# Optimization experiments

Hardware: AMD Instinct MI355X
Metric: run time of the kernel (lower is better)

## Reference

```python
import jax, jax.numpy as jnp
import numpy as np

B, H, W, C = 8, 64, 64, 64
C8 = C // 8

def setup_inputs() -> dict:
    key = jax.random.key(0)
    ks = jax.random.split(key, 5)
    x = jax.random.normal(ks[0], (B, H, W, C), dtype=jnp.float32)
    # 1x1 conv kernels (fan-in scaled) + biases
    wq = jax.random.normal(ks[1], (C, C8), dtype=jnp.float32) / np.sqrt(C)
    wk = jax.random.normal(ks[2], (C, C8), dtype=jnp.float32) / np.sqrt(C)
    wv = jax.random.normal(ks[3], (C, C), dtype=jnp.float32) / np.sqrt(C)
    bq = jnp.zeros((C8,), dtype=jnp.float32)
    bk = jnp.zeros((C8,), dtype=jnp.float32)
    bv = jnp.zeros((C,), dtype=jnp.float32)
    gamma = jax.random.normal(ks[4], (), dtype=jnp.float32)
    return {"x": x, "wq": wq, "bq": bq, "wk": wk, "bk": bk,
            "wv": wv, "bv": bv, "gamma": gamma}

def reference(x, wq, bq, wk, bk, wv, bv, gamma):
    b, h, w, c = x.shape
    n = h * w
    # 1x1 convs == per-pixel linear projections
    q = (jnp.einsum('bhwc,cd->bhwd', x, wq) + bq).reshape(b, n, -1)  # [B,N,C/8]
    k = (jnp.einsum('bhwc,cd->bhwd', x, wk) + bk).reshape(b, n, -1)  # [B,N,C/8]
    v = (jnp.einsum('bhwc,cd->bhwd', x, wv) + bv).reshape(b, n, -1)  # [B,N,C]
    # Unscaled attention: softmax over keys (last axis), no 1/sqrt(d)
    attn = jax.nn.softmax(jnp.einsum('bnd,bmd->bnm', q, k), axis=-1)  # [B,N,N]
    out = jnp.einsum('bnm,bmc->bnc', attn, v).reshape(b, h, w, c)
    return out * gamma + x
```

## Files before the change

kernel.cpp:

```cpp
#include <hip/hip_runtime.h>
#include <hip/hip_bf16.h>


#define BB 8
#define NN 4096
#define CC 64
#define PSTRIDE 72
#define LOG2E 1.44269504088896f

typedef _Float16 f16;
typedef _Float16 half8 __attribute__((ext_vector_type(8)));
typedef _Float16 half4 __attribute__((ext_vector_type(4)));
typedef __fp16 fp16x2 __attribute__((ext_vector_type(2)));
typedef float floatx4 __attribute__((ext_vector_type(4)));

static __device__ inline half4 pack4(float a, float b, float c, float d) {
    fp16x2 lo = __builtin_amdgcn_cvt_pkrtz(a, b);
    fp16x2 hi = __builtin_amdgcn_cvt_pkrtz(c, d);
    unsigned int lou = __builtin_bit_cast(unsigned int, lo);
    unsigned int hiu = __builtin_bit_cast(unsigned int, hi);
    unsigned long long packed = (unsigned long long)lou | ((unsigned long long)hiu << 32);
    return __builtin_bit_cast(half4, packed);
}


__global__ __launch_bounds__(256) void proj_all_kernel(
    const float* __restrict__ x,
    const float* __restrict__ wq, const float* __restrict__ bq,
    const float* __restrict__ wk, const float* __restrict__ bk,
    const float* __restrict__ wv, const float* __restrict__ bv,
    f16* __restrict__ Qh, f16* __restrict__ Kf, f16* __restrict__ Vf,
    float* __restrict__ qn2, float* __restrict__ kn2)
{
    __shared__ alignas(16) f16 Ws[80][PSTRIDE];
    __shared__ float Bs[80];
    __shared__ alignas(16) f16 Vs[64][68];
    __shared__ alignas(16) f16 Ks[64][12];
    const int tid = threadIdx.x;

    for (int i = tid; i < 4096; i += 256) {
        int cin = i >> 6, cout = i & 63;
        Ws[cout][cin] = (f16)wv[i];
    }
    for (int i = tid; i < 512; i += 256) {
        int cin = i >> 3, c = i & 7;
        Ws[64 + c][cin] = (f16)(wq[i] * LOG2E);
        Ws[72 + c][cin] = (f16)wk[i];
    }
    if (tid < 80)
        Bs[tid] = (tid < 64) ? bv[tid]
                : (tid < 72 ? bq[tid - 64] * LOG2E : bk[tid - 72]);
    __syncthreads();

    const int wave = tid >> 6, lane = tid & 63;
    const int quad = lane >> 4, n16 = lane & 15;
    const long pb = (long)blockIdx.x * 64;
    const long p0 = pb + wave * 16;
    const int  b   = (int)(pb >> 12);
    const int  nnb = (int)(pb & 4095);

    half8 ax[2];
#pragma unroll
    for (int kh = 0; kh < 2; ++kh) {
        const float* xp = x + (p0 + n16) * 64 + kh * 32 + quad * 8;
        float4 x1 = *(const float4*)xp;
        float4 x2 = *(const float4*)(xp + 4);
        ax[kh][0] = (f16)x1.x; ax[kh][1] = (f16)x1.y;
        ax[kh][2] = (f16)x1.z; ax[kh][3] = (f16)x1.w;
        ax[kh][4] = (f16)x2.x; ax[kh][5] = (f16)x2.y;
        ax[kh][6] = (f16)x2.z; ax[kh][7] = (f16)x2.w;
    }

#pragma unroll
    for (int ct = 0; ct < 5; ++ct) {
        const int cout = (ct < 4) ? ct * 16 + n16 : 64 + n16;
        const float bias = Bs[cout];
        half8 b0 = *(const half8*)(&Ws[cout][quad * 8]);
        half8 b1 = *(const half8*)(&Ws[cout][32 + quad * 8]);
        floatx4 acc = {bias, bias, bias, bias};
        acc = __builtin_amdgcn_mfma_f32_16x16x32_f16(ax[0], b0, acc, 0, 0, 0);
        acc = __builtin_amdgcn_mfma_f32_16x16x32_f16(ax[1], b1, acc, 0, 0, 0);
        if (ct < 4) {
#pragma unroll
            for (int r = 0; r < 4; ++r)
                Vs[wave * 16 + quad * 4 + r][ct * 16 + n16] = (f16)acc[r];
        } else {
            float n2[4];
#pragma unroll
            for (int r = 0; r < 4; ++r) n2[r] = acc[r] * acc[r];
#pragma unroll
            for (int d = 1; d < 8; d <<= 1)
#pragma unroll
                for (int r = 0; r < 4; ++r) n2[r] += __shfl_xor(n2[r], d, 64);
            if (n16 == 0) {
#pragma unroll
                for (int r = 0; r < 4; ++r) qn2[p0 + quad * 4 + r] = n2[r];
            } else if (n16 == 8) {
#pragma unroll
                for (int r = 0; r < 4; ++r) kn2[p0 + quad * 4 + r] = n2[r];
            }
            if (n16 < 8) {
                f16* dst = Qh + (p0 + quad * 4) * 8 + n16;
#pragma unroll
                for (int r = 0; r < 4; ++r) dst[r * 8] = (f16)acc[r];
            } else {
#pragma unroll
                for (int r = 0; r < 4; ++r)
                    Ks[wave * 16 + quad * 4 + r][n16 - 8] = (f16)acc[r];
            }
        }
    }
    __syncthreads();

#pragma unroll
    for (int u = 0; u < 2; ++u) {
        const int tt = wave * 2 + u;
        const int kb = tt >> 2, ct = tt & 3;
        half8 v;
#pragma unroll
        for (int j = 0; j < 4; ++j)
            v[j] = Vs[kb * 32 + quad * 4 + j][ct * 16 + n16];
#pragma unroll
        for (int j = 0; j < 4; ++j)
            v[4 + j] = Vs[kb * 32 + 16 + quad * 4 + j][ct * 16 + n16];
        const size_t kbg = (size_t)b * 128 + (nnb >> 5) + kb;
        *(half8*)(Vf + (kbg * 4 + ct) * 512 + lane * 8) = v;
    }
    if (wave < 2) {
        half8 kp;
#pragma unroll
        for (int e = 0; e < 2; ++e) {
            const int t = wave * 2 + e;
#pragma unroll
            for (int j = 0; j < 4; ++j) {
                f16 v = (f16)0.f;
                if (quad < 2) v = Ks[t * 16 + n16][quad * 4 + j];
                else if (quad == 2 && j == 0) v = (f16)1.f;
                kp[e * 4 + j] = v;
            }
        }
        const size_t kpg = (size_t)b * 128 + (nnb >> 5) + wave;
        *(half8*)(Kf + kpg * 512 + lane * 8) = kp;
    }
}

__global__ __launch_bounds__(256) void knorm_max_kernel(
    const float* __restrict__ kn2, float* __restrict__ Mk2)
{
    __shared__ float red[4];
    const int b = blockIdx.x, tid = threadIdx.x;
    float mx = 0.f;
    for (int i = tid; i < NN; i += 256) mx = fmaxf(mx, kn2[(size_t)b * NN + i]);
#pragma unroll
    for (int d = 1; d < 64; d <<= 1) mx = fmaxf(mx, __shfl_xor(mx, d, 64));
    if ((tid & 63) == 0) red[tid >> 6] = mx;
    __syncthreads();
    if (tid == 0) Mk2[b] = fmaxf(fmaxf(red[0], red[1]), fmaxf(red[2], red[3]));
}

__global__ __launch_bounds__(256, 2) void attn_kernel(
    const f16* __restrict__ Qh, const f16* __restrict__ Kf,
    const f16* __restrict__ Vf,
    const float* __restrict__ qn2, const float* __restrict__ Mk2,
    const float* __restrict__ x, const float* __restrict__ gptr,
    float* __restrict__ out)
{
    __shared__ alignas(16) float Obuf[3 * 4 * 64 * 20];
    __shared__ float Ls[4][4][16];

    const int tid  = threadIdx.x;
    const int wave = tid >> 6, lane = tid & 63;
    const int quad = lane >> 4, n16 = lane & 15;
    const int ks = wave;

    const int b  = blockIdx.x & 7;
    const int qt = blockIdx.x >> 3;
    const size_t bN = (size_t)b * NN;

    const float mk2 = Mk2[b];

    half4 bq4[4];
#pragma unroll
    for (int qs = 0; qs < 4; ++qs) {
        const int q = qt * 64 + qs * 16 + n16;
        const float mf = __builtin_sqrtf(qn2[bN + q] * mk2) - 12.0f;
        half4 v = {0, 0, 0, 0};
        if (quad < 2)
            v = *(const half4*)(Qh + (bN + q) * 8 + quad * 4);
        else if (quad == 2)
            v[0] = (f16)(-mf);
        bq4[qs] = v;
    }

    floatx4 oacc[4][4];
#pragma unroll
    for (int qs = 0; qs < 4; ++qs)
#pragma unroll
        for (int ct = 0; ct < 4; ++ct) oacc[qs][ct] = (floatx4){0.f, 0.f, 0.f, 0.f};
    float l_loc[4] = {0.f, 0.f, 0.f, 0.f};

    const f16* kfb = Kf + ((size_t)b * 128 + ks * 32) * 512 + lane * 8;
    const f16* vfb = Vf + ((size_t)b * 128 + ks * 32) * 2048 + lane * 8;
    const floatx4 zero4 = {0.f, 0.f, 0.f, 0.f};

    half8 kkc0 = *(const half8*)(kfb + 0);
    half8 kkc1 = *(const half8*)(kfb + 512);

    for (int it = 0; it < 16; ++it) {
        half8 avp[2][4];
#pragma unroll
        for (int p = 0; p < 2; ++p)
#pragma unroll
            for (int ct = 0; ct < 4; ++ct)
                avp[p][ct] = *(const half8*)(vfb + ((size_t)(it * 2 + p) * 4 + ct) * 512);

        half4 ak[4];
        ak[0] = __builtin_shufflevector(kkc0, kkc0, 0, 1, 2, 3);
        ak[1] = __builtin_shufflevector(kkc0, kkc0, 4, 5, 6, 7);
        ak[2] = __builtin_shufflevector(kkc1, kkc1, 0, 1, 2, 3);
        ak[3] = __builtin_shufflevector(kkc1, kkc1, 4, 5, 6, 7);

        const int itn = (it < 15) ? it + 1 : 15;
        kkc0 = *(const half8*)(kfb + (size_t)itn * 1024);
        kkc1 = *(const half8*)(kfb + (size_t)itn * 1024 + 512);

#pragma unroll
        for (int qs = 0; qs < 4; ++qs) {
            floatx4 sf[4];
#pragma unroll
            for (int t = 0; t < 4; ++t)
                sf[t] = __builtin_amdgcn_mfma_f32_16x16x16f16(ak[t], bq4[qs], zero4, 0, 0, 0);

            half4 pk[4];
            float rst[4];
#pragma unroll
            for (int t = 0; t < 4; ++t) {
                float p0 = __builtin_exp2f(sf[t][0]);
                float p1 = __builtin_exp2f(sf[t][1]);
                float p2 = __builtin_exp2f(sf[t][2]);
                float p3 = __builtin_exp2f(sf[t][3]);
                rst[t] = (p0 + p1) + (p2 + p3);
                pk[t] = pack4(p0, p1, p2, p3);
            }
            l_loc[qs] += (rst[0] + rst[1]) + (rst[2] + rst[3]);

#pragma unroll
            for (int t = 0; t < 4; ++t) {
                const int p = t >> 1;
#pragma unroll
                for (int ct = 0; ct < 4; ++ct) {
                    half4 va = (t & 1)
                        ? __builtin_shufflevector(avp[p][ct], avp[p][ct], 4, 5, 6, 7)
                        : __builtin_shufflevector(avp[p][ct], avp[p][ct], 0, 1, 2, 3);
                    oacc[qs][ct] = __builtin_amdgcn_mfma_f32_16x16x16f16(va, pk[t], oacc[qs][ct], 0, 0, 0);
                }
            }
        }
    }

    float l_run[4];
#pragma unroll
    for (int qs = 0; qs < 4; ++qs) {
        float l = l_loc[qs];
        l += __shfl_xor(l, 16, 64);
        l += __shfl_xor(l, 32, 64);
        l_run[qs] = l;
    }

    __syncthreads();
    if (ks > 0) {
#pragma unroll
        for (int qs = 0; qs < 4; ++qs) {
            if (quad == 0) Ls[ks][qs][n16] = l_run[qs];
            float* ob = Obuf + (size_t)(((ks - 1) * 4 + qs) * 64 + lane) * 20;
#pragma unroll
            for (int ct = 0; ct < 4; ++ct)
                *(floatx4*)(ob + ct * 4) = oacc[qs][ct];
        }
    }
    __syncthreads();
    if (ks == 0) {
        const float g = gptr[0];
#pragma unroll
        for (int qs = 0; qs < 4; ++qs) {
            float l = l_run[qs];
#pragma unroll
            for (int p = 1; p < 4; ++p) {
                l += Ls[p][qs][n16];
                const float* ob = Obuf + (size_t)(((p - 1) * 4 + qs) * 64 + lane) * 20;
#pragma unroll
                for (int ct = 0; ct < 4; ++ct) {
                    floatx4 t = *(const floatx4*)(ob + ct * 4);
                    oacc[qs][ct] += t;
                }
            }
            const float scale = g / l;
            const int q = qt * 64 + qs * 16 + n16;
#pragma unroll
            for (int ct = 0; ct < 4; ++ct) {
                const size_t idx = (bN + q) * CC + ct * 16 + quad * 4;
                float4 xr = *(const float4*)(x + idx);
                float4 res;
                res.x = oacc[qs][ct][0] * scale + xr.x;
                res.y = oacc[qs][ct][1] * scale + xr.y;
                res.z = oacc[qs][ct][2] * scale + xr.z;
                res.w = oacc[qs][ct][3] * scale + xr.w;
                *(float4*)(out + idx) = res;
            }
        }
    }
}

extern "C" void kernel_launch(void* const* d_in, const int* in_sizes, int n_in,
                              void* d_out, int out_size, void* d_ws, size_t ws_size,
                              hipStream_t stream) {
    const float* x     = (const float*)d_in[0];
    const float* wq    = (const float*)d_in[1];
    const float* bq    = (const float*)d_in[2];
    const float* wk    = (const float*)d_in[3];
    const float* bk    = (const float*)d_in[4];
    const float* wv    = (const float*)d_in[5];
    const float* bv    = (const float*)d_in[6];
    const float* gamma = (const float*)d_in[7];
    float* out = (float*)d_out;

    f16* Qh = (f16*)d_ws;
    f16* Kf = Qh + (size_t)BB * NN * 8;
    f16* Vf = Kf + (size_t)BB * 128 * 512;
    float* qn2 = (float*)(Vf + (size_t)BB * 128 * 4 * 512);
    float* kn2 = qn2 + (size_t)BB * NN;
    float* Mk2 = kn2 + (size_t)BB * NN;

    proj_all_kernel<<<512, 256, 0, stream>>>(x, wq, bq, wk, bk, wv, bv,
                                             Qh, Kf, Vf, qn2, kn2);
    knorm_max_kernel<<<BB, 256, 0, stream>>>(kn2, Mk2);
    attn_kernel<<<BB * 64, 256, 0, stream>>>(Qh, Kf, Vf, qn2, Mk2, x, gamma, out);
}
```

Measured before the change: 131.0 us.

## Shrink attention block to 16 queries for higher occupancy and more blocks

Each attention block now handles 16 queries instead of 64, so the grid grows fourfold to 2048 blocks. Launch bounds rise to 8 blocks per SM, and the accumulator registers and shared reduction buffer shrink to match. The aim is better latency hiding through occupancy and a more even spread of work across CUs. The cost is that K and V are loaded from memory four times as often, since each K/V tile is now reused across only 16 queries instead of 64.

New measurement: 172.3 us. 31.5% more time.

```diff
diff --git a/kernel.cpp b/kernel.cpp
--- a/kernel.cpp
+++ b/kernel.cpp
@@ -158,15 +158,15 @@
     if (tid == 0) Mk2[b] = fmaxf(fmaxf(red[0], red[1]), fmaxf(red[2], red[3]));
 }
 
-__global__ __launch_bounds__(256, 2) void attn_kernel(
+__global__ __launch_bounds__(256, 8) void attn_kernel(
     const f16* __restrict__ Qh, const f16* __restrict__ Kf,
     const f16* __restrict__ Vf,
     const float* __restrict__ qn2, const float* __restrict__ Mk2,
     const float* __restrict__ x, const float* __restrict__ gptr,
     float* __restrict__ out)
 {
-    __shared__ alignas(16) float Obuf[3 * 4 * 64 * 20];
-    __shared__ float Ls[4][4][16];
+    __shared__ alignas(16) float Obuf[3 * 64 * 20];
+    __shared__ float Ls[4][16];
 
     const int tid  = threadIdx.x;
     const int wave = tid >> 6, lane = tid & 63;
@@ -179,25 +179,22 @@
 
     const float mk2 = Mk2[b];
 
-    half4 bq4[4];
-#pragma unroll
-    for (int qs = 0; qs < 4; ++qs) {
-        const int q = qt * 64 + qs * 16 + n16;
+    half4 bq4;
+    {
+        const int q = qt * 16 + n16;
         const float mf = __builtin_sqrtf(qn2[bN + q] * mk2) - 12.0f;
         half4 v = {0, 0, 0, 0};
         if (quad < 2)
             v = *(const half4*)(Qh + (bN + q) * 8 + quad * 4);
         else if (quad == 2)
             v[0] = (f16)(-mf);
-        bq4[qs] = v;
-    }
-
-    floatx4 oacc[4][4];
-#pragma unroll
-    for (int qs = 0; qs < 4; ++qs)
-#pragma unroll
-        for (int ct = 0; ct < 4; ++ct) oacc[qs][ct] = (floatx4){0.f, 0.f, 0.f, 0.f};
-    float l_loc[4] = {0.f, 0.f, 0.f, 0.f};
+        bq4 = v;
+    }
+
+    floatx4 oacc[4];
+#pragma unroll
+    for (int ct = 0; ct < 4; ++ct) oacc[ct] = (floatx4){0.f, 0.f, 0.f, 0.f};
+    float l_loc = 0.f;
 
     const f16* kfb = Kf + ((size_t)b * 128 + ks * 32) * 512 + lane * 8;
     const f16* vfb = Vf + ((size_t)b * 128 + ks * 32) * 2048 + lane * 8;
@@ -207,13 +204,6 @@
     half8 kkc1 = *(const half8*)(kfb + 512);
 
     for (int it = 0; it < 16; ++it) {
-        half8 avp[2][4];
-#pragma unroll
-        for (int p = 0; p < 2; ++p)
-#pragma unroll
-            for (int ct = 0; ct < 4; ++ct)
-                avp[p][ct] = *(const half8*)(vfb + ((size_t)(it * 2 + p) * 4 + ct) * 512);
-
         half4 ak[4];
         ak[0] = __builtin_shufflevector(kkc0, kkc0, 0, 1, 2, 3);
         ak[1] = __builtin_shufflevector(kkc0, kkc0, 4, 5, 6, 7);
@@ -225,88 +215,75 @@
         kkc1 = *(const half8*)(kfb + (size_t)itn * 1024 + 512);
 
 #pragma unroll
-        for (int qs = 0; qs < 4; ++qs) {
-            floatx4 sf[4];
-#pragma unroll
-            for (int t = 0; t < 4; ++t)
-                sf[t] = __builtin_amdgcn_mfma_f32_16x16x16f16(ak[t], bq4[qs], zero4, 0, 0, 0);
-
-            half4 pk[4];
-            float rst[4];
-#pragma unroll
-            for (int t = 0; t < 4; ++t) {
-                float p0 = __builtin_exp2f(sf[t][0]);
-                float p1 = __builtin_exp2f(sf[t][1]);
-                float p2 = __builtin_exp2f(sf[t][2]);
-                float p3 = __builtin_exp2f(sf[t][3]);
-                rst[t] = (p0 + p1) + (p2 + p3);
-                pk[t] = pack4(p0, p1, p2, p3);
-            }
-            l_loc[qs] += (rst[0] + rst[1]) + (rst[2] + rst[3]);
-
-#pragma unroll
-            for (int t = 0; t < 4; ++t) {
-                const int p = t >> 1;
+        for (int p = 0; p < 2; ++p) {
+            half8 av[4];
+#pragma unroll
+            for (int ct = 0; ct < 4; ++ct)
+                av[ct] = *(const half8*)(vfb + ((size_t)(it * 2 + p) * 4 + ct) * 512);
+
+#pragma unroll
+            for (int e = 0; e < 2; ++e) {
+                const int t = p * 2 + e;
+                floatx4 sf = __builtin_amdgcn_mfma_f32_16x16x16f16(ak[t], bq4, zero4, 0, 0, 0);
+                float p0 = __builtin_exp2f(sf[0]);
+                float p1 = __builtin_exp2f(sf[1]);
+                float p2 = __builtin_exp2f(sf[2]);
+                float p3 = __builtin_exp2f(sf[3]);
+                l_loc += (p0 + p1) + (p2 + p3);
+                half4 pk = pack4(p0, p1, p2, p3);
 #pragma unroll
                 for (int ct = 0; ct < 4; ++ct) {
-                    half4 va = (t & 1)
-                        ? __builtin_shufflevector(avp[p][ct], avp[p][ct], 4, 5, 6, 7)
-                        : __builtin_shufflevector(avp[p][ct], avp[p][ct], 0, 1, 2, 3);
-                    oacc[qs][ct] = __builtin_amdgcn_mfma_f32_16x16x16f16(va, pk[t], oacc[qs][ct], 0, 0, 0);
+                    half4 va = e
+                        ? __builtin_shufflevector(av[ct], av[ct], 4, 5, 6, 7)
+                        : __builtin_shufflevector(av[ct], av[ct], 0, 1, 2, 3);
+                    oacc[ct] = __builtin_amdgcn_mfma_f32_16x16x16f16(va, pk, oacc[ct], 0, 0, 0);
                 }
             }
         }
     }
 
-    float l_run[4];
-#pragma unroll
-    for (int qs = 0; qs < 4; ++qs) {
-        float l = l_loc[qs];
+    float l_run;
+    {
+        float l = l_loc;
         l += __shfl_xor(l, 16, 64);
         l += __shfl_xor(l, 32, 64);
-        l_run[qs] = l;
+        l_run = l;
     }
 
     __syncthreads();
     if (ks > 0) {
-#pragma unroll
-        for (int qs = 0; qs < 4; ++qs) {
-            if (quad == 0) Ls[ks][qs][n16] = l_run[qs];
-            float* ob = Obuf + (size_t)(((ks - 1) * 4 + qs) * 64 + lane) * 20;
-#pragma unroll
-            for (int ct = 0; ct < 4; ++ct)
-                *(floatx4*)(ob + ct * 4) = oacc[qs][ct];
-        }
+        if (quad == 0) Ls[ks][n16] = l_run;
+        float* ob = Obuf + (size_t)((ks - 1) * 64 + lane) * 20;
+#pragma unroll
+        for (int ct = 0; ct < 4; ++ct)
+            *(floatx4*)(ob + ct * 4) = oacc[ct];
     }
     __syncthreads();
     if (ks == 0) {
         const float g = gptr[0];
-#pragma unroll
-        for (int qs = 0; qs < 4; ++qs) {
-            float l = l_run[qs];
-#pragma unroll
-            for (int p = 1; p < 4; ++p) {
-                l += Ls[p][qs][n16];
-                const float* ob = Obuf + (size_t)(((p - 1) * 4 + qs) * 64 + lane) * 20;
-#pragma unroll
-                for (int ct = 0; ct < 4; ++ct) {
-                    floatx4 t = *(const floatx4*)(ob + ct * 4);
-                    oacc[qs][ct] += t;
-                }
-            }
-            const float scale = g / l;
-            const int q = qt * 64 + qs * 16 + n16;
+        float l = l_run;
+#pragma unroll
+        for (int p = 1; p < 4; ++p) {
+            l += Ls[p][n16];
+            const float* ob = Obuf + (size_t)((p - 1) * 64 + lane) * 20;
 #pragma unroll
             for (int ct = 0; ct < 4; ++ct) {
-                const size_t idx = (bN + q) * CC + ct * 16 + quad * 4;
-                float4 xr = *(const float4*)(x + idx);
-                float4 res;
-                res.x = oacc[qs][ct][0] * scale + xr.x;
-                res.y = oacc[qs][ct][1] * scale + xr.y;
-                res.z = oacc[qs][ct][2] * scale + xr.z;
-                res.w = oacc[qs][ct][3] * scale + xr.w;
-                *(float4*)(out + idx) = res;
-            }
+                floatx4 t = *(const floatx4*)(ob + ct * 4);
+                oacc[ct] += t;
+            }
+        }
+        const float scale = g / l;
+        const int q = qt * 16 + n16;
+#pragma unroll
+        for (int ct = 0; ct < 4; ++ct) {
+            const size_t idx = (bN + q) * CC + ct * 16 + quad * 4;
+            float4 xr = *(const float4*)(x + idx);
+            float4 res;
+            res.x = oacc[ct][0] * scale + xr.x;
+            res.y = oacc[ct][1] * scale + xr.y;
+            res.z = oacc[ct][2] * scale + xr.z;
+            res.w = oacc[ct][3] * scale + xr.w;
+            *(float4*)(out + idx) = res;
         }
     }
 }
@@ -334,5 +311,5 @@
     proj_all_kernel<<<512, 256, 0, stream>>>(x, wq, bq, wk, bk, wv, bv,
                                              Qh, Kf, Vf, qn2, kn2);
     knorm_max_kernel<<<BB, 256, 0, stream>>>(kn2, Mk2);
-    attn_kernel<<<BB * 64, 256, 0, stream>>>(Qh, Kf, Vf, qn2, Mk2, x, gamma, out);
-}
+    attn_kernel<<<BB * 256, 256, 0, stream>>>(Qh, Kf, Vf, qn2, Mk2, x, gamma, out);
+}
```
